# Optimization experiments

Hardware: AMD Instinct MI355X
Metric: run time of the kernel (lower is better)

## Reference

```python
import jax, jax.numpy as jnp
import numpy as np

EMBED_DIM = 1024
BATCH = 4
SEQ = 2048


def setup_inputs() -> dict:
    key = jax.random.key(0)
    ks = jax.random.split(key, 9)
    D = EMBED_DIM
    s = 1.0 / np.sqrt(D)
    inputs = jax.random.normal(ks[0], (BATCH, SEQ, D), dtype=jnp.float32)
    rotation_params = jax.random.normal(ks[1], (D, D), dtype=jnp.float32) * s
    entangle_params = jax.random.normal(ks[2], (D, D), dtype=jnp.float32) * s
    Wq = jax.random.normal(ks[3], (D, D), dtype=jnp.float32) * s
    bq = jax.random.normal(ks[4], (D,), dtype=jnp.float32) * 0.01
    Wk = jax.random.normal(ks[5], (D, D), dtype=jnp.float32) * s
    bk = jax.random.normal(ks[6], (D,), dtype=jnp.float32) * 0.01
    Wv = jax.random.normal(ks[7], (D, D), dtype=jnp.float32) * s
    bv = jax.random.normal(ks[8], (D,), dtype=jnp.float32) * 0.01
    # causal mask: True = masked out (matches torch masked_fill semantics)
    mask = jnp.triu(jnp.ones((SEQ, SEQ), dtype=bool), k=1)
    return {"inputs": inputs, "rotation_params": rotation_params,
            "entangle_params": entangle_params, "Wq": Wq, "bq": bq,
            "Wk": Wk, "bk": bk, "Wv": Wv, "bv": bv, "mask": mask}


def reference(inputs, rotation_params, entangle_params, Wq, bq, Wk, bk, Wv, bv, mask):
    D = inputs.shape[-1]
    # q = Linear(x) @ R^T ; k = Linear(x) @ E^T ; v = Linear(x)
    q = (jnp.einsum('bsd,ed->bse', inputs, Wq) + bq) @ rotation_params.T
    k = (jnp.einsum('bsd,ed->bse', inputs, Wk) + bk) @ entangle_params.T
    v = jnp.einsum('bsd,ed->bse', inputs, Wv) + bv
    scores = jnp.einsum('bqd,bkd->bqk', q, k) / jnp.sqrt(jnp.float32(D))
    scores = jnp.where(mask, jnp.float32(-jnp.inf), scores)
    probs = jax.nn.softmax(scores, axis=-1)  # dropout=0.0 -> identity
    return jnp.einsum('bqk,bkd->bqd', probs, v)
```

## Files before the change

### kernel.cpp

```cpp
#include <hip/hip_runtime.h>
#include <hip/hip_bf16.h>
#include <stdint.h>
#include <math.h>

#define DD 1024
#define SS 2048
#define BB 4

typedef __bf16 bf16;
typedef __bf16 bf16x8 __attribute__((ext_vector_type(8)));
typedef __bf16 bf16x4 __attribute__((ext_vector_type(4)));
typedef float f32x4 __attribute__((ext_vector_type(4)));

__device__ __forceinline__ void gload_lds16(const bf16* g, bf16* l) {
  __builtin_amdgcn_global_load_lds(
      (const __attribute__((address_space(1))) void*)g,
      (__attribute__((address_space(3))) void*)l, 16, 0, 0);
}

__global__ __launch_bounds__(256) void prep_all(
    const float* __restrict__ x, const float* __restrict__ R,
    const float* __restrict__ E, const float* __restrict__ Wv,
    const float* __restrict__ Wq, const float* __restrict__ Wk,
    const float* __restrict__ bq, const float* __restrict__ bk,
    const float* __restrict__ bv, bf16* __restrict__ xb,
    bf16* __restrict__ Rb, bf16* __restrict__ Eb, bf16* __restrict__ Wvb,
    bf16* __restrict__ WqT, bf16* __restrict__ WkT, float* __restrict__ bias,
    float* __restrict__ rowsums) {
  int bid = blockIdx.x;
  int t = threadIdx.x;
  if (bid < 11264) {
    const float* src;
    bf16* dst;
    int base;
    if (bid < 8192) { src = x; dst = xb; base = bid; }
    else if (bid < 9216) { src = R; dst = Rb; base = bid - 8192; }
    else if (bid < 10240) { src = E; dst = Eb; base = bid - 9216; }
    else { src = Wv; dst = Wvb; base = bid - 10240; }
    int i = (base * 256 + t) * 4;
    float4 v = *(const float4*)(src + i);
    bf16x4 o;
    o.x = (bf16)v.x; o.y = (bf16)v.y; o.z = (bf16)v.z; o.w = (bf16)v.w;
    *(bf16x4*)(dst + i) = o;
  } else if (bid < 13312) {
    int r2 = bid - 11264;
    const float* src = (r2 >= 1024) ? Wk : Wq;
    bf16* dst = (r2 >= 1024) ? WkT : WqT;
    int rem = r2 & 1023;
    int bx = rem & 31, by = rem >> 5;
    __shared__ float tile[32][33];
    int tx = t & 31, ty = t >> 5;
    int xcol = bx * 32 + tx;
    int y0 = by * 32;
    for (int r = ty; r < 32; r += 8)
      tile[r][tx] = src[(y0 + r) * DD + xcol];
    __syncthreads();
    int dx = by * 32 + tx;
    int dy0 = bx * 32;
    for (int r = ty; r < 32; r += 8)
      dst[(dy0 + r) * DD + dx] = (bf16)tile[tx][r];
  } else if (bid < 16384) {
    int e = bid - 13312;
    if (e >= 2048) { if (t == 0) bias[e] = bv[e - 2048]; return; }
    const float* M = (e < 1024) ? R : E;
    const float* bb = (e < 1024) ? bq : bk;
    int row = e & 1023;
    float s = 0.f;
    for (int f = t; f < DD; f += 256) s += M[row * DD + f] * bb[f];
    for (int o = 32; o >= 1; o >>= 1) s += __shfl_xor(s, o, 64);
    __shared__ float red[4];
    if ((t & 63) == 0) red[t >> 6] = s;
    __syncthreads();
    if (t == 0) bias[e] = red[0] + red[1] + red[2] + red[3];
  } else {
    int idx = (bid - 16384) * 256 + t;
    rowsums[idx] = 0.f;
  }
}

template <int MODE>
__global__ __launch_bounds__(256, 4)
void gemm_bt(const bf16* __restrict__ Ag, long lda, long sAb,
             const bf16* __restrict__ Bg, long ldb, long sBb,
             void* __restrict__ Cg, long ldc, long sCb,
             const float* __restrict__ bias, float scale, int K,
             bf16* __restrict__ vTp, float* __restrict__ rowsums) {
  __shared__ __align__(16) bf16 smem[16384];
  bf16* As = smem;
  bf16* Bs = smem + 8192;

  int bx = blockIdx.x, by = blockIdx.y, bz = blockIdx.z;
  if (MODE == 1) {
    int q = bx;
    by = (int)((sqrtf(8.f * q + 1.f) - 1.f) * 0.5f);
    while ((by + 1) * (by + 2) / 2 <= q) by++;
    while (by * (by + 1) / 2 > q) by--;
    bx = q - by * (by + 1) / 2;
  }
  if (MODE == 2) by = 15 - by;
  long m0 = (long)by * 128, n0 = (long)bx * 128;
  const bf16* A = Ag + (long)bz * sAb + m0 * lda;
  const bf16* Bp = Bg + (long)bz * sBb + n0 * ldb;

  int t = threadIdx.x;
  int w = t >> 6, l = t & 63;
  int lr = l >> 2;
  int lc = (((l & 3) ^ (lr & 3)) * 8);
  int quad = l >> 4, ln = l & 15;
  int wm = w >> 1, wn = w & 1;
  int rdoff = ((quad ^ (ln & 3)) * 8);

  int Keff = (MODE == 2) ? (by + 1) * 128 : K;

  f32x4 acc[4][4];
#pragma unroll
  for (int i = 0; i < 4; i++)
#pragma unroll
    for (int j = 0; j < 4; j++) acc[i][j] = f32x4{0.f, 0.f, 0.f, 0.f};

  const bf16* a_base = As + (wm * 64 + ln) * 32 + rdoff;
  const bf16* b_base = Bs + (wn * 64 + ln) * 32 + rdoff;
  long arow0 = (long)(w * 16 + lr);

  for (int k0 = 0; k0 < Keff; k0 += 64) {
#pragma unroll
    for (int kk = 0; kk < 2; kk++) {
      int kc = k0 + kk * 32 + lc;
      gload_lds16(A + arow0 * lda + kc, As + kk * 4096 + w * 512);
      gload_lds16(A + (arow0 + 64) * lda + kc, As + kk * 4096 + 2048 + w * 512);
      gload_lds16(Bp + arow0 * ldb + kc, Bs + kk * 4096 + w * 512);
      gload_lds16(Bp + (arow0 + 64) * ldb + kc, Bs + kk * 4096 + 2048 + w * 512);
    }
    asm volatile("s_waitcnt vmcnt(0)" ::: "memory");
    __syncthreads();

#pragma unroll
    for (int kk = 0; kk < 2; kk++) {
      bf16x8 af[4], bfr[4];
#pragma unroll
      for (int i = 0; i < 4; i++) {
        af[i] = *(const bf16x8*)(a_base + kk * 4096 + i * 512);
        bfr[i] = *(const bf16x8*)(b_base + kk * 4096 + i * 512);
      }
#pragma unroll
      for (int i = 0; i < 4; i++)
#pragma unroll
        for (int j = 0; j < 4; j++)
          acc[i][j] = __builtin_amdgcn_mfma_f32_16x16x32_bf16(
              af[i], bfr[j], acc[i][j], 0, 0, 0);
    }
    __syncthreads();
  }

  if (MODE == 0) {
    if (vTp && n0 >= 2048) {
      int d0 = (int)n0 - 2048;
      int b = (int)(m0 >> 11);
      int s0 = (int)(m0 & 2047);
#pragma unroll
      for (int i = 0; i < 4; i++) {
        int sb = wm * 64 + i * 16 + quad * 4;
#pragma unroll
        for (int j = 0; j < 4; j++) {
          int d = wn * 64 + j * 16 + ln;
          float bv_ = bias[n0 + d];
#pragma unroll
          for (int r = 0; r < 4; r++)
            smem[d * 128 + ((sb + r) ^ (ln << 3))] = (bf16)(acc[i][j][r] + bv_);
        }
      }
      __syncthreads();
      int d = t >> 1, h = t & 1;
      bf16* dst = vTp + (long)b * DD * SS + (long)(d0 + d) * SS + s0 + h * 64;
#pragma unroll
      for (int j = 0; j < 8; j++) {
        int sbase = h * 64 + j * 8;
        bf16x8 v = *(const bf16x8*)(smem + d * 128 + (sbase ^ ((d & 15) << 3)));
        *(bf16x8*)(dst + j * 8) = v;
      }
    } else {
      bf16* C = (bf16*)Cg + (long)bz * sCb + m0 * ldc + n0;
#pragma unroll
      for (int i = 0; i < 4; i++) {
        int rb = wm * 64 + i * 16 + quad * 4;
#pragma unroll
        for (int j = 0; j < 4; j++) {
          int col = wn * 64 + j * 16 + ln;
          float bv_ = bias ? bias[n0 + col] : 0.f;
#pragma unroll
          for (int r = 0; r < 4; r++)
            C[(long)(rb + r) * ldc + col] = (bf16)(acc[i][j][r] + bv_);
        }
      }
    }
  } else if (MODE == 1) {
#pragma unroll
    for (int i = 0; i < 4; i++) {
      int rb = wm * 64 + i * 16 + quad * 4;
#pragma unroll
      for (int j = 0; j < 4; j++) {
        int col = wn * 64 + j * 16 + ln;
#pragma unroll
        for (int r = 0; r < 4; r++) {
          int row = rb + r;
          float p = 0.f;
          if (n0 + col <= m0 + row) p = __expf(acc[i][j][r] * scale);
          smem[row * 128 + (col ^ ((row & 15) << 3))] = (bf16)p;
        }
      }
    }
    __syncthreads();
    int row = t >> 1, h = t & 1;
    bf16* P = (bf16*)Cg + (long)bz * sCb + (m0 + row) * ldc + n0;
    float rsum = 0.f;
#pragma unroll
    for (int jj = 0; jj < 8; jj++) {
      int p8 = h * 8 + jj;
      int slot = p8 ^ (row & 15);
      bf16x8 v = *(const bf16x8*)(smem + row * 128 + slot * 8);
#pragma unroll
      for (int e = 0; e < 8; e++) rsum += (float)v[e];
      *(bf16x8*)(P + p8 * 8) = v;
    }
    atomicAdd(&rowsums[(long)bz * SS + m0 + row], rsum);
  } else {
    float* C = (float*)Cg + (long)bz * sCb + m0 * ldc + n0;
    const float* rs = rowsums + (long)bz * SS + m0;
#pragma unroll
    for (int i = 0; i < 4; i++) {
      int rb = wm * 64 + i * 16 + quad * 4;
      float inv[4];
#pragma unroll
      for (int r = 0; r < 4; r++) inv[r] = 1.f / rs[rb + r];
#pragma unroll
      for (int j = 0; j < 4; j++) {
        int col = wn * 64 + j * 16 + ln;
#pragma unroll
        for (int r = 0; r < 4; r++)
          C[(long)(rb + r) * ldc + col] = acc[i][j][r] * inv[r];
      }
    }
  }
}

extern "C" void kernel_launch(void* const* d_in, const int* in_sizes, int n_in,
                              void* d_out, int out_size, void* d_ws,
                              size_t ws_size, hipStream_t stream) {
  const float* x = (const float*)d_in[0];
  const float* R = (const float*)d_in[1];
  const float* E = (const float*)d_in[2];
  const float* Wq = (const float*)d_in[3];
  const float* bq = (const float*)d_in[4];
  const float* Wk = (const float*)d_in[5];
  const float* bk = (const float*)d_in[6];
  const float* Wv = (const float*)d_in[7];
  const float* bv = (const float*)d_in[8];
  float* out = (float*)d_out;

  char* ws = (char*)d_ws;
  bf16* qkv = (bf16*)ws;
  bf16* vT = (bf16*)(ws + 50331648);
  bf16* probs = (bf16*)(ws + 67108864);
  float* rowsums = (float*)(ws + 100663296);
  char* sr = ws + 101711872;
  bf16* xb = (bf16*)sr;
  bf16* Rb = (bf16*)(sr + 16777216);
  bf16* Eb = Rb + 1024 * 1024;
  bf16* WqT = (bf16*)(sr + 20971520);
  bf16* WkT = WqT + 1024 * 1024;
  bf16* wcat = (bf16*)(sr + 25165824);
  float* bias = (float*)(sr + 31457280);

  prep_all<<<16416, 256, 0, stream>>>(x, R, E, Wv, Wq, Wk, bq, bk, bv, xb, Rb,
                                      Eb, wcat + 2048 * DD, WqT, WkT, bias,
                                      rowsums);

  gemm_bt<0><<<dim3(8, 8, 2), 256, 0, stream>>>(
      Rb, DD, 1024 * 1024, WqT, DD, 1024 * 1024, wcat, DD, 1024 * 1024,
      nullptr, 1.f, DD, nullptr, nullptr);

  gemm_bt<0><<<dim3(24, 64, 1), 256, 0, stream>>>(xb, DD, 0, wcat, DD, 0, qkv,
                                                  3072, 0, bias, 1.f, DD, vT,
                                                  nullptr);

  gemm_bt<1><<<dim3(136, 1, BB), 256, 0, stream>>>(
      qkv, 3072, (long)SS * 3072, qkv + 1024, 3072, (long)SS * 3072, probs,
      SS, (long)SS * SS, nullptr, 0.03125f, DD, nullptr, rowsums);

  gemm_bt<2><<<dim3(8, 16, BB), 256, 0, stream>>>(
      probs, SS, (long)SS * SS, vT, SS, (long)DD * SS, out,
      DD, (long)SS * DD, nullptr, 1.f, SS, nullptr, rowsums);
}
```

Before: 303.2 us.

## Double-buffer GEMM K-loop with async LDS prefetch and XCD-aware tile remap

The GEMM main loop moves from a 64-wide K step with two barriers to a 32-wide double-buffered pipeline. The next K slice is issued into the other LDS buffer before the MFMAs on the current one, so global loads overlap compute and one barrier per step is dropped. It also remaps workgroup IDs for the projection and score GEMMs so consecutive tiles land on the same XCD, aiming for better L2 reuse. The trade-off is more iterations, each with a full vmcnt(0) wait and barrier. The prefetch is only waited on at the next iteration, so any LDS hazard depends on the barrier placement being correct.

```diff
diff --git a/kernel.cpp b/kernel.cpp
--- a/kernel.cpp
+++ b/kernel.cpp
@@ -90,6 +90,17 @@
   bf16* Bs = smem + 8192;
 
   int bx = blockIdx.x, by = blockIdx.y, bz = blockIdx.z;
+  if (MODE == 0 || MODE == 1) {
+    int nx = (int)gridDim.x;
+    int nwg = nx * (int)gridDim.y;
+    int id = by * nx + bx;
+    int xcd = id & 7, rest = id >> 3;
+    int q8 = nwg >> 3, r8 = nwg & 7;
+    int wg = (xcd < r8 ? xcd * (q8 + 1) : r8 * (q8 + 1) + (xcd - r8) * q8)
+             + rest;
+    bx = wg % nx;
+    by = wg / nx;
+  }
   if (MODE == 1) {
     int q = bx;
     by = (int)((sqrtf(8.f * q + 1.f) - 1.f) * 0.5f);
@@ -122,35 +133,40 @@
   const bf16* b_base = Bs + (wn * 64 + ln) * 32 + rdoff;
   long arow0 = (long)(w * 16 + lr);
 
-  for (int k0 = 0; k0 < Keff; k0 += 64) {
-#pragma unroll
-    for (int kk = 0; kk < 2; kk++) {
-      int kc = k0 + kk * 32 + lc;
-      gload_lds16(A + arow0 * lda + kc, As + kk * 4096 + w * 512);
-      gload_lds16(A + (arow0 + 64) * lda + kc, As + kk * 4096 + 2048 + w * 512);
-      gload_lds16(Bp + arow0 * ldb + kc, Bs + kk * 4096 + w * 512);
-      gload_lds16(Bp + (arow0 + 64) * ldb + kc, Bs + kk * 4096 + 2048 + w * 512);
-    }
+#define STG(p, kc0)                                                         \
+  {                                                                         \
+    int kc = (kc0) + lc;                                                    \
+    gload_lds16(A + arow0 * lda + kc, As + (p) * 4096 + w * 512);           \
+    gload_lds16(A + (arow0 + 64) * lda + kc,                                \
+                As + (p) * 4096 + 2048 + w * 512);                          \
+    gload_lds16(Bp + arow0 * ldb + kc, Bs + (p) * 4096 + w * 512);          \
+    gload_lds16(Bp + (arow0 + 64) * ldb + kc,                               \
+                Bs + (p) * 4096 + 2048 + w * 512);                          \
+  }
+
+  STG(0, 0);
+  int cur = 0;
+  for (int k = 0; k < Keff; k += 32) {
     asm volatile("s_waitcnt vmcnt(0)" ::: "memory");
-    __syncthreads();
-
-#pragma unroll
-    for (int kk = 0; kk < 2; kk++) {
-      bf16x8 af[4], bfr[4];
-#pragma unroll
-      for (int i = 0; i < 4; i++) {
-        af[i] = *(const bf16x8*)(a_base + kk * 4096 + i * 512);
-        bfr[i] = *(const bf16x8*)(b_base + kk * 4096 + i * 512);
-      }
-#pragma unroll
-      for (int i = 0; i < 4; i++)
-#pragma unroll
-        for (int j = 0; j < 4; j++)
-          acc[i][j] = __builtin_amdgcn_mfma_f32_16x16x32_bf16(
-              af[i], bfr[j], acc[i][j], 0, 0, 0);
-    }
-    __syncthreads();
-  }
+    __builtin_amdgcn_s_barrier();
+    __builtin_amdgcn_sched_barrier(0);
+    if (k + 32 < Keff) STG(cur ^ 1, k + 32);
+    bf16x8 af[4], bfr[4];
+#pragma unroll
+    for (int i = 0; i < 4; i++) {
+      af[i] = *(const bf16x8*)(a_base + cur * 4096 + i * 512);
+      bfr[i] = *(const bf16x8*)(b_base + cur * 4096 + i * 512);
+    }
+#pragma unroll
+    for (int i = 0; i < 4; i++)
+#pragma unroll
+      for (int j = 0; j < 4; j++)
+        acc[i][j] = __builtin_amdgcn_mfma_f32_16x16x32_bf16(
+            af[i], bfr[j], acc[i][j], 0, 0, 0);
+    cur ^= 1;
+  }
+#undef STG
+  __syncthreads();
 
   if (MODE == 0) {
     if (vTp && n0 >= 2048) {
```

Measured after the change: 298.1 us. No clear change (-1.7%).
